# Optimization experiments

Hardware: AMD Instinct MI355X
Metric: run time of the kernel (lower is better)

The kernel has to match this reference:

```python
import jax, jax.numpy as jnp
import numpy as np

NUM_EXPERTS = 8
TOP_K = 2


def setup_inputs() -> dict:
    key = jax.random.key(0)
    k1, k2 = jax.random.split(key)
    N, D = 8192, 4096
    inputs = jax.random.normal(k1, (N, D), dtype=jnp.float32)
    # torch.nn.Linear weight is [out_features, in_features] = [E, D]
    gate_w = jax.random.normal(k2, (NUM_EXPERTS, D), dtype=jnp.float32) * (1.0 / np.sqrt(D))
    return {"inputs": inputs, "gate_w": gate_w}


def reference(inputs, gate_w):
    # gate linear (no bias): [N, D] x [D, E] -> [N, E]
    router_logits = jnp.einsum("nd,ed->ne", inputs.astype(jnp.float32), gate_w)
    router_weights = jax.nn.softmax(router_logits, axis=1)
    # top-k over experts, renormalize selected weights
    sel_w, sel_idx = jax.lax.top_k(router_weights, TOP_K)          # [N, K]
    sel_w = sel_w / jnp.sum(sel_w, axis=-1, keepdims=True)
    # dense equivalent of the per-expert torch.where dispatch:
    # combine[n, e] = renormalized weight of token n for expert e (0 if not selected).
    onehot = jax.nn.one_hot(sel_idx, NUM_EXPERTS, dtype=sel_w.dtype)  # [N, K, E]
    combine = jnp.einsum("nk,nke->ne", sel_w, onehot)               # [N, E]
    return combine, sel_idx
```

## Files before the change

kernel.cpp:

```cpp
#include <hip/hip_runtime.h>
#include <math.h>

#define N_TOK 8192
#define DIM   4096
#define NEXP  8
#define TPW   4
#define HALF  (DIM / 2)
#define ITERS (HALF / 256)

__global__ __launch_bounds__(256) void router_kernel(
    const float* __restrict__ x,
    const float* __restrict__ w,
    float* __restrict__ out)
{
    __shared__ float red[2][TPW][NEXP];

    const int lane   = threadIdx.x & 63;
    const int waveid = threadIdx.x >> 6;
    const int g      = waveid >> 1;
    const int h      = waveid & 1;
    const int n0     = blockIdx.x * 8 + g * TPW;

    float acc[TPW][NEXP];
    #pragma unroll
    for (int t = 0; t < TPW; ++t)
        #pragma unroll
        for (int e = 0; e < NEXP; ++e) acc[t][e] = 0.0f;

    const int dbase = h * HALF + lane * 4;
    const float* xr = x + (size_t)n0 * DIM + dbase;
    const float* wr = w + dbase;

    float4 xb[3][TPW];
    #pragma unroll
    for (int t = 0; t < TPW; ++t)
        xb[0][t] = *(const float4*)(xr + (size_t)t * DIM);
    #pragma unroll
    for (int t = 0; t < TPW; ++t)
        xb[1][t] = *(const float4*)(xr + (size_t)t * DIM + 256);

    #pragma unroll
    for (int it = 0; it < ITERS; ++it) {
        if (it + 2 < ITERS) {
            const int off = (it + 2) * 256;
            #pragma unroll
            for (int t = 0; t < TPW; ++t)
                xb[(it + 2) % 3][t] = *(const float4*)(xr + (size_t)t * DIM + off);
        }

        float4 wv[NEXP];
        #pragma unroll
        for (int e = 0; e < NEXP; ++e)
            wv[e] = *(const float4*)(wr + (size_t)e * DIM + it * 256);

        #pragma unroll
        for (int t = 0; t < TPW; ++t) {
            const float4 xv = xb[it % 3][t];
            #pragma unroll
            for (int e = 0; e < NEXP; ++e) {
                acc[t][e] = fmaf(xv.x, wv[e].x,
                            fmaf(xv.y, wv[e].y,
                            fmaf(xv.z, wv[e].z,
                            fmaf(xv.w, wv[e].w, acc[t][e]))));
            }
        }
    }

    #pragma unroll
    for (int t = 0; t < TPW; ++t) {
        #pragma unroll
        for (int e = 0; e < NEXP; ++e) {
            float v = acc[t][e];
            #pragma unroll
            for (int off = 32; off >= 1; off >>= 1)
                v += __shfl_xor(v, off, 64);
            acc[t][e] = v;
        }
    }

    if (h == 1 && lane == 0) {
        #pragma unroll
        for (int t = 0; t < TPW; ++t) {
            *(float4*)&red[g][t][0] = make_float4(acc[t][0], acc[t][1], acc[t][2], acc[t][3]);
            *(float4*)&red[g][t][4] = make_float4(acc[t][4], acc[t][5], acc[t][6], acc[t][7]);
        }
    }
    __syncthreads();

    if (h == 0) {
        #pragma unroll
        for (int t = 0; t < TPW; ++t) {
            float4 r0 = *(const float4*)&red[g][t][0];
            float4 r1 = *(const float4*)&red[g][t][4];
            acc[t][0] += r0.x; acc[t][1] += r0.y; acc[t][2] += r0.z; acc[t][3] += r0.w;
            acc[t][4] += r1.x; acc[t][5] += r1.y; acc[t][6] += r1.z; acc[t][7] += r1.w;
        }

        #pragma unroll
        for (int t = 0; t < TPW; ++t) {
            float m1 = acc[t][0]; int i1 = 0;
            #pragma unroll
            for (int e = 1; e < NEXP; ++e)
                if (acc[t][e] > m1) { m1 = acc[t][e]; i1 = e; }
            float m2 = -INFINITY; int i2 = 0;
            #pragma unroll
            for (int e = 0; e < NEXP; ++e)
                if (e != i1 && acc[t][e] > m2) { m2 = acc[t][e]; i2 = e; }

            const float e2  = expf(m2 - m1);
            const float inv = 1.0f / (1.0f + e2);
            const float w1  = inv;
            const float w2  = e2 * inv;

            if (lane == 0) {
                const int n = n0 + t;
                float c[8];
                #pragma unroll
                for (int e = 0; e < 8; ++e)
                    c[e] = (e == i1) ? w1 : ((e == i2) ? w2 : 0.0f);
                float4* cp = (float4*)(out + (size_t)n * 8);
                cp[0] = make_float4(c[0], c[1], c[2], c[3]);
                cp[1] = make_float4(c[4], c[5], c[6], c[7]);
                float* ip = out + (size_t)N_TOK * 8 + (size_t)n * 2;
                ip[0] = (float)i1;
                ip[1] = (float)i2;
            }
        }
    }
}

extern "C" void kernel_launch(void* const* d_in, const int* in_sizes, int n_in,
                              void* d_out, int out_size, void* d_ws, size_t ws_size,
                              hipStream_t stream) {
    const float* x = (const float*)d_in[0];
    const float* w = (const float*)d_in[1];
    float* out = (float*)d_out;

    dim3 grid(N_TOK / 8);
    dim3 block(256);
    hipLaunchKernelGGL(router_kernel, grid, block, 0, stream, x, w, out);
}
```

Before: 32.99 us.

## Split router into partial-dot kernel with LDS-staged weights and separate top-2 kernel

The GEMV is restructured so that each block handles 16 tokens over half of the hidden dimension. The block stages its half of the gate weights in shared memory and preloads all x values into registers up front instead of using a rolling prefetch. Partial logits go to the workspace and a second small kernel sums the two halves and does the top-2 softmax. This removes repeated global weight loads and the in-block cross-wave reduction. The cost is an extra launch, a workspace round trip, 64KB of LDS per block that limits occupancy, and high register pressure from holding all x values at once.

Result: no change. 33.01 us (+0.0%).

```diff
diff --git a/kernel.cpp b/kernel.cpp
--- a/kernel.cpp
+++ b/kernel.cpp
@@ -7,19 +7,43 @@
 #define TPW   4
 #define HALF  (DIM / 2)
 #define ITERS (HALF / 256)
-
-__global__ __launch_bounds__(256) void router_kernel(
+#define WS_NEED ((size_t)N_TOK * 2 * NEXP * sizeof(float))
+
+__global__ __launch_bounds__(256) void router_part_kernel(
     const float* __restrict__ x,
     const float* __restrict__ w,
-    float* __restrict__ out)
+    float* __restrict__ part)
 {
-    __shared__ float red[2][TPW][NEXP];
-
-    const int lane   = threadIdx.x & 63;
-    const int waveid = threadIdx.x >> 6;
-    const int g      = waveid >> 1;
-    const int h      = waveid & 1;
-    const int n0     = blockIdx.x * 8 + g * TPW;
+    __shared__ float wl[NEXP][HALF];
+
+    const int tid  = threadIdx.x;
+    const int lane = tid & 63;
+    const int wid  = tid >> 6;
+    const int h    = blockIdx.x & 1;
+    const int blk  = blockIdx.x >> 1;
+    const int n0   = blk * 16 + wid * TPW;
+
+    {
+        const float* wsrc = w + h * HALF;
+        #pragma unroll
+        for (int e = 0; e < NEXP; ++e) {
+            #pragma unroll
+            for (int p = 0; p < 2; ++p) {
+                const int pos = p * 1024 + tid * 4;
+                const float4 v = *(const float4*)(wsrc + (size_t)e * DIM + pos);
+                *(float4*)&wl[e][pos] = v;
+            }
+        }
+    }
+    __syncthreads();
+
+    const float* xr = x + (size_t)n0 * DIM + h * HALF + lane * 4;
+    float4 xq[ITERS][TPW];
+    #pragma unroll
+    for (int j = 0; j < ITERS; ++j)
+        #pragma unroll
+        for (int t = 0; t < TPW; ++t)
+            xq[j][t] = *(const float4*)(xr + (size_t)t * DIM + j * 256);
 
     float acc[TPW][NEXP];
     #pragma unroll
@@ -27,35 +51,15 @@
         #pragma unroll
         for (int e = 0; e < NEXP; ++e) acc[t][e] = 0.0f;
 
-    const int dbase = h * HALF + lane * 4;
-    const float* xr = x + (size_t)n0 * DIM + dbase;
-    const float* wr = w + dbase;
-
-    float4 xb[3][TPW];
-    #pragma unroll
-    for (int t = 0; t < TPW; ++t)
-        xb[0][t] = *(const float4*)(xr + (size_t)t * DIM);
-    #pragma unroll
-    for (int t = 0; t < TPW; ++t)
-        xb[1][t] = *(const float4*)(xr + (size_t)t * DIM + 256);
-
-    #pragma unroll
-    for (int it = 0; it < ITERS; ++it) {
-        if (it + 2 < ITERS) {
-            const int off = (it + 2) * 256;
-            #pragma unroll
-            for (int t = 0; t < TPW; ++t)
-                xb[(it + 2) % 3][t] = *(const float4*)(xr + (size_t)t * DIM + off);
-        }
-
+    #pragma unroll
+    for (int j = 0; j < ITERS; ++j) {
         float4 wv[NEXP];
         #pragma unroll
         for (int e = 0; e < NEXP; ++e)
-            wv[e] = *(const float4*)(wr + (size_t)e * DIM + it * 256);
-
-        #pragma unroll
-        for (int t = 0; t < TPW; ++t) {
-            const float4 xv = xb[it % 3][t];
+            wv[e] = *(const float4*)&wl[e][j * 256 + lane * 4];
+        #pragma unroll
+        for (int t = 0; t < TPW; ++t) {
+            const float4 xv = xq[j][t];
             #pragma unroll
             for (int e = 0; e < NEXP; ++e) {
                 acc[t][e] = fmaf(xv.x, wv[e].x,
@@ -78,6 +82,112 @@
         }
     }
 
+    if (lane == 0) {
+        #pragma unroll
+        for (int t = 0; t < TPW; ++t) {
+            float* p = part + ((size_t)(n0 + t) * 2 + h) * NEXP;
+            *(float4*)(p + 0) = make_float4(acc[t][0], acc[t][1], acc[t][2], acc[t][3]);
+            *(float4*)(p + 4) = make_float4(acc[t][4], acc[t][5], acc[t][6], acc[t][7]);
+        }
+    }
+}
+
+__global__ __launch_bounds__(256) void router_top2_kernel(
+    const float* __restrict__ part,
+    float* __restrict__ out)
+{
+    const int n = blockIdx.x * 256 + threadIdx.x;
+    const float4* p = (const float4*)(part + (size_t)n * 16);
+    const float4 a = p[0], b = p[1];
+    const float4 c = p[2], d = p[3];
+
+    float l[NEXP];
+    l[0] = a.x + c.x; l[1] = a.y + c.y; l[2] = a.z + c.z; l[3] = a.w + c.w;
+    l[4] = b.x + d.x; l[5] = b.y + d.y; l[6] = b.z + d.z; l[7] = b.w + d.w;
+
+    float m1 = l[0]; int i1 = 0;
+    #pragma unroll
+    for (int e = 1; e < NEXP; ++e)
+        if (l[e] > m1) { m1 = l[e]; i1 = e; }
+    float m2 = -INFINITY; int i2 = 0;
+    #pragma unroll
+    for (int e = 0; e < NEXP; ++e)
+        if (e != i1 && l[e] > m2) { m2 = l[e]; i2 = e; }
+
+    const float e2  = expf(m2 - m1);
+    const float inv = 1.0f / (1.0f + e2);
+    const float w1  = inv;
+    const float w2  = e2 * inv;
+
+    float cmb[8];
+    #pragma unroll
+    for (int e = 0; e < 8; ++e)
+        cmb[e] = (e == i1) ? w1 : ((e == i2) ? w2 : 0.0f);
+    float4* cp = (float4*)(out + (size_t)n * 8);
+    cp[0] = make_float4(cmb[0], cmb[1], cmb[2], cmb[3]);
+    cp[1] = make_float4(cmb[4], cmb[5], cmb[6], cmb[7]);
+    float* ip = out + (size_t)N_TOK * 8 + (size_t)n * 2;
+    ip[0] = (float)i1;
+    ip[1] = (float)i2;
+}
+
+__global__ __launch_bounds__(256) void router_fallback_kernel(
+    const float* __restrict__ x, const float* __restrict__ w,
+    float* __restrict__ out)
+{
+    __shared__ float red[2][TPW][NEXP];
+    const int lane = threadIdx.x & 63;
+    const int wid  = threadIdx.x >> 6;
+    const int g    = wid >> 1;
+    const int h    = wid & 1;
+    const int n0   = blockIdx.x * 8 + g * TPW;
+
+    float acc[TPW][NEXP];
+    #pragma unroll
+    for (int t = 0; t < TPW; ++t)
+        #pragma unroll
+        for (int e = 0; e < NEXP; ++e) acc[t][e] = 0.0f;
+
+    const int dbase = h * HALF + lane * 4;
+    const float* xr = x + (size_t)n0 * DIM + dbase;
+    const float* wr = w + dbase;
+
+    float4 xb[3][TPW];
+    #pragma unroll
+    for (int t = 0; t < TPW; ++t) xb[0][t] = *(const float4*)(xr + (size_t)t * DIM);
+    #pragma unroll
+    for (int t = 0; t < TPW; ++t) xb[1][t] = *(const float4*)(xr + (size_t)t * DIM + 256);
+
+    #pragma unroll
+    for (int it = 0; it < ITERS; ++it) {
+        if (it + 2 < ITERS) {
+            const int off = (it + 2) * 256;
+            #pragma unroll
+            for (int t = 0; t < TPW; ++t)
+                xb[(it + 2) % 3][t] = *(const float4*)(xr + (size_t)t * DIM + off);
+        }
+        float4 wv[NEXP];
+        #pragma unroll
+        for (int e = 0; e < NEXP; ++e)
+            wv[e] = *(const float4*)(wr + (size_t)e * DIM + it * 256);
+        #pragma unroll
+        for (int t = 0; t < TPW; ++t) {
+            const float4 xv = xb[it % 3][t];
+            #pragma unroll
+            for (int e = 0; e < NEXP; ++e)
+                acc[t][e] = fmaf(xv.x, wv[e].x, fmaf(xv.y, wv[e].y,
+                            fmaf(xv.z, wv[e].z, fmaf(xv.w, wv[e].w, acc[t][e]))));
+        }
+    }
+    #pragma unroll
+    for (int t = 0; t < TPW; ++t)
+        #pragma unroll
+        for (int e = 0; e < NEXP; ++e) {
+            float v = acc[t][e];
+            #pragma unroll
+            for (int off = 32; off >= 1; off >>= 1) v += __shfl_xor(v, off, 64);
+            acc[t][e] = v;
+        }
     if (h == 1 && lane == 0) {
         #pragma unroll
         for (int t = 0; t < TPW; ++t) {
@@ -86,7 +196,6 @@
         }
     }
     __syncthreads();
-
     if (h == 0) {
         #pragma unroll
         for (int t = 0; t < TPW; ++t) {
@@ -95,7 +204,6 @@
             acc[t][0] += r0.x; acc[t][1] += r0.y; acc[t][2] += r0.z; acc[t][3] += r0.w;
             acc[t][4] += r1.x; acc[t][5] += r1.y; acc[t][6] += r1.z; acc[t][7] += r1.w;
         }
-
         #pragma unroll
         for (int t = 0; t < TPW; ++t) {
             float m1 = acc[t][0]; int i1 = 0;
@@ -106,18 +214,14 @@
             #pragma unroll
             for (int e = 0; e < NEXP; ++e)
                 if (e != i1 && acc[t][e] > m2) { m2 = acc[t][e]; i2 = e; }
-
             const float e2  = expf(m2 - m1);
             const float inv = 1.0f / (1.0f + e2);
-            const float w1  = inv;
-            const float w2  = e2 * inv;
-
             if (lane == 0) {
                 const int n = n0 + t;
                 float c[8];
                 #pragma unroll
                 for (int e = 0; e < 8; ++e)
-                    c[e] = (e == i1) ? w1 : ((e == i2) ? w2 : 0.0f);
+                    c[e] = (e == i1) ? inv : ((e == i2) ? e2 * inv : 0.0f);
                 float4* cp = (float4*)(out + (size_t)n * 8);
                 cp[0] = make_float4(c[0], c[1], c[2], c[3]);
                 cp[1] = make_float4(c[4], c[5], c[6], c[7]);
@@ -136,7 +240,14 @@
     const float* w = (const float*)d_in[1];
     float* out = (float*)d_out;
 
-    dim3 grid(N_TOK / 8);
-    dim3 block(256);
-    hipLaunchKernelGGL(router_kernel, grid, block, 0, stream, x, w, out);
-}
+    if (ws_size >= WS_NEED) {
+        float* part = (float*)d_ws;
+        hipLaunchKernelGGL(router_part_kernel, dim3(1024), dim3(256), 0, stream,
+                           x, w, part);
+        hipLaunchKernelGGL(router_top2_kernel, dim3(N_TOK / 256), dim3(256), 0, stream,
+                           part, out);
+    } else {
+        hipLaunchKernelGGL(router_fallback_kernel, dim3(N_TOK / 8), dim3(256), 0, stream,
+                           x, w, out);
+    }
+}
```
